# Performance work log

Measured on AMD Instinct MI355X. Metric: run time of the kernel, lower is better.

## Reference

```python
import jax, jax.numpy as jnp
import numpy as np

N_NODES = 100000
N_EDGES = 1600000
N_FEAT = 128
HIDDEN = 128
N_GRAPHS = 100


def setup_inputs() -> dict:
    key = jax.random.key(0)
    ks = jax.random.split(key, 12)
    glorot = lambda k, fi, fo: jax.random.normal(k, (fo, fi), jnp.float32) * (1.0 / np.sqrt(fi))
    x = jax.random.normal(ks[0], (N_NODES, N_FEAT), jnp.float32)
    edge_index = jax.random.randint(ks[1], (2, N_EDGES), 0, N_NODES, jnp.int64)
    batch = jnp.sort(jax.random.randint(ks[2], (N_NODES,), 0, N_GRAPHS, jnp.int64))
    return {
        "x": x,
        "edge_index": edge_index,
        "batch": batch,
        "W1": glorot(ks[3], N_FEAT, HIDDEN), "b1": jnp.zeros((HIDDEN,), jnp.float32),
        "W2": glorot(ks[4], HIDDEN, HIDDEN), "b2": jnp.zeros((HIDDEN,), jnp.float32),
        "W3": glorot(ks[5], HIDDEN, HIDDEN), "b3": jnp.zeros((HIDDEN,), jnp.float32),
        "W4": glorot(ks[6], HIDDEN, HIDDEN), "b4": jnp.zeros((HIDDEN,), jnp.float32),
    }


def _aggregate(x, edge_index):
    # GIN aggregation with eps=0: (1+eps)*x_i + sum_{j in N(i)} x_j
    src, dst = edge_index[0], edge_index[1]
    agg = jax.ops.segment_sum(x[src], dst, num_segments=N_NODES)
    return x + agg


def _mlp(h, Wa, ba, Wb, bb):
    h = jax.nn.relu(h @ Wa.T + ba)
    return jax.nn.relu(h @ Wb.T + bb)


def reference(x, edge_index, batch, W1, b1, W2, b2, W3, b3, W4, b4):
    # conv1: GINConv(MLP1), then extra relu (no-op after MLP's relu), dropout in eval = identity
    h = _mlp(_aggregate(x, edge_index), W1, b1, W2, b2)
    # conv2: GINConv(MLP2), then relu
    h = _mlp(_aggregate(h, edge_index), W3, b3, W4, b4)
    # global mean pool over graphs
    sums = jax.ops.segment_sum(h, batch, num_segments=N_GRAPHS)
    counts = jax.ops.segment_sum(jnp.ones((h.shape[0],), h.dtype), batch, num_segments=N_GRAPHS)
    x_pool = sums / jnp.maximum(counts, 1.0)[:, None]
    return (x_pool, h)
```

## Files before the change

kernel.cpp:

```cpp
#include <hip/hip_runtime.h>

#define N_NODES  100000
#define N_EDGES  1600000
#define NF       128
#define N_GRAPHS 100
#define NBKT     391
#define BKT_SHIFT 8
#define CAP      6144
#define EPB      4096
#define EB_GRID  391

typedef __attribute__((ext_vector_type(8))) short bf16x8;
typedef __attribute__((ext_vector_type(4))) float f32x4;
typedef unsigned int uint32;

__device__ __forceinline__ unsigned short f2bf(float f) {
    union { float f; uint32 u; } x; x.f = f;
    return (unsigned short)((x.u + 0x7fffu + ((x.u >> 16) & 1u)) >> 16);
}
__device__ __forceinline__ uint32 pack2bf(float a, float b) {
    union { float f; uint32 u; } x, y; x.f = a; y.f = b;
    uint32 lo = (x.u + 0x7fffu + ((x.u >> 16) & 1u)) >> 16;
    uint32 hi = (y.u + 0x7fffu + ((y.u >> 16) & 1u)) & 0xffff0000u;
    return lo | hi;
}
__device__ __forceinline__ void add_bf8(float* acc, uint4 v) {
    uint32 u[4] = {v.x, v.y, v.z, v.w};
    #pragma unroll
    for (int i = 0; i < 4; ++i) {
        union { uint32 b; float f; } lo, hi;
        lo.b = u[i] << 16; hi.b = u[i] & 0xffff0000u;
        acc[2 * i] += lo.f; acc[2 * i + 1] += hi.f;
    }
}

__global__ __launch_bounds__(256) void prep(const float4* __restrict__ x,
                                            const float4* __restrict__ w1,
                                            const float4* __restrict__ w2,
                                            const float4* __restrict__ w3,
                                            const float4* __restrict__ w4,
                                            uint4* __restrict__ xb, uint4* __restrict__ wb,
                                            int* __restrict__ cur, float* __restrict__ sums) {
    int bid = blockIdx.x, t = threadIdx.x;
    if (bid < 6250) {
        int i = bid * 256 + t;
        float4 a = x[i * 2], b = x[i * 2 + 1];
        uint4 o;
        o.x = pack2bf(a.x, a.y); o.y = pack2bf(a.z, a.w);
        o.z = pack2bf(b.x, b.y); o.w = pack2bf(b.z, b.w);
        xb[i] = o;
    } else if (bid < 6282) {
        int i = (bid - 6250) * 256 + t;
        int wi = i >> 11, li = i & 2047;
        const float4* s = (wi == 0) ? w1 : (wi == 1) ? w2 : (wi == 2) ? w3 : w4;
        float4 a = s[li * 2], b = s[li * 2 + 1];
        uint4 o;
        o.x = pack2bf(a.x, a.y); o.y = pack2bf(a.z, a.w);
        o.z = pack2bf(b.x, b.y); o.w = pack2bf(b.z, b.w);
        wb[i] = o;
    } else {
        int idx = (bid - 6282) * 256 + t;
        for (int i = idx; i < N_GRAPHS * NF; i += 4096) sums[i] = 0.f;
        if (idx < NBKT) cur[idx] = 0;
    }
}

__global__ __launch_bounds__(512) void bscatter(const int* __restrict__ src,
                                                const int* __restrict__ dst,
                                                int* __restrict__ cur,
                                                uint32* __restrict__ ebuf) {
    __shared__ int lh[NBKT], lbase[NBKT];
    int t = threadIdx.x;
    if (t < NBKT) lh[t] = 0;
    __syncthreads();
    int e0 = blockIdx.x * EPB;
    int d[8];
    #pragma unroll
    for (int i = 0; i < 8; ++i) {
        int e = e0 + i * 512 + t;
        d[i] = -1;
        if (e < N_EDGES) { d[i] = dst[e]; atomicAdd(&lh[d[i] >> BKT_SHIFT], 1); }
    }
    __syncthreads();
    if (t < NBKT) { lbase[t] = t * CAP + atomicAdd(&cur[t], lh[t]); lh[t] = 0; }
    __syncthreads();
    #pragma unroll
    for (int i = 0; i < 8; ++i) {
        int e = e0 + i * 512 + t;
        if (e < N_EDGES) {
            int b = d[i] >> BKT_SHIFT;
            int off = atomicAdd(&lh[b], 1);
            ebuf[lbase[b] + off] = ((uint32)(d[i] & 255) << 17) | (uint32)src[e];
        }
    }
}

__global__ __launch_bounds__(256) void bfine(const uint32* __restrict__ ebuf,
                                             const int* __restrict__ cur,
                                             int* __restrict__ rowptr,
                                             int* __restrict__ rowend,
                                             int* __restrict__ csr) {
    __shared__ int deg[256], off[256];
    int t = threadIdx.x;
    int bkt = blockIdx.x;
    int beg = bkt * CAP;
    int end = beg + cur[bkt];
    deg[t] = 0;
    __syncthreads();
    for (int e = beg + t; e < end; e += 256)
        atomicAdd(&deg[ebuf[e] >> 17], 1);
    __syncthreads();
    int d = deg[t];
    off[t] = d;
    __syncthreads();
    for (int o = 1; o < 256; o <<= 1) {
        int x = (t >= o) ? off[t - o] : 0;
        __syncthreads();
        off[t] += x;
        __syncthreads();
    }
    int ex = off[t] - d;
    int node = (bkt << BKT_SHIFT) + t;
    if (node < N_NODES) { rowptr[node] = beg + ex; rowend[node] = beg + ex + d; }
    __syncthreads();
    off[t] = ex;
    __syncthreads();
    for (int e = beg + t; e < end; e += 256) {
        uint32 u = ebuf[e];
        int pos = atomicAdd(&off[u >> 17], 1);
        csr[beg + pos] = (int)(u & 0x1FFFFu);
    }
}

__global__ __launch_bounds__(256) void gather_agg_bf16(const uint4* __restrict__ x,
                                                       const int* __restrict__ rowptr,
                                                       const int* __restrict__ rowend,
                                                       const int* __restrict__ csr,
                                                       uint4* __restrict__ out) {
    int gid  = blockIdx.x * 256 + threadIdx.x;
    int node = gid >> 6;
    int l = threadIdx.x & 63;
    int c = l & 15;
    int j = l >> 4;
    int beg = rowptr[node], end = rowend[node];

    float acc[8];
    #pragma unroll
    for (int i = 0; i < 8; ++i) acc[i] = 0.f;

    for (int e = beg; e < end; e += 16) {
        int s[4];
        #pragma unroll
        for (int k = 0; k < 4; ++k) {
            int ee = min(e + j + 4 * k, end - 1);
            s[k] = csr[ee];
        }
        uint4 v[4];
        #pragma unroll
        for (int k = 0; k < 4; ++k) v[k] = x[s[k] * 16 + c];
        #pragma unroll
        for (int k = 0; k < 4; ++k)
            if (e + j + 4 * k < end) add_bf8(acc, v[k]);
    }

    #pragma unroll
    for (int i = 0; i < 8; ++i) {
        acc[i] += __shfl_xor(acc[i], 16, 64);
        acc[i] += __shfl_xor(acc[i], 32, 64);
    }

    add_bf8(acc, x[node * 16 + c]);

    if (j == 0) {
        uint4 o;
        o.x = pack2bf(acc[0], acc[1]); o.y = pack2bf(acc[2], acc[3]);
        o.z = pack2bf(acc[4], acc[5]); o.w = pack2bf(acc[6], acc[7]);
        out[node * 16 + c] = o;
    }
}

template <bool F32OUT>
__global__ __launch_bounds__(256, 4) void mlp_mfma(const unsigned short* __restrict__ A,
                                                   const unsigned short* __restrict__ Wa,
                                                   const float* __restrict__ ba,
                                                   const unsigned short* __restrict__ Wb,
                                                   const float* __restrict__ bb,
                                                   void* __restrict__ Cout, int M) {
    __shared__ unsigned short Mid[128 * 136];
    int tid  = threadIdx.x;
    int row0 = blockIdx.x * 128;
    int wv = tid >> 6, l = tid & 63, lm = l & 15, q = l >> 4;

    const unsigned short* pa0 = A + (size_t)min(row0 + wv * 32 + lm,      M - 1) * NF;
    const unsigned short* pa1 = A + (size_t)min(row0 + wv * 32 + 16 + lm, M - 1) * NF;
    const unsigned short* pwa = Wa + lm * NF;
    const unsigned short* pwb = Wb + lm * NF;

    f32x4 acc[2][8];
    #pragma unroll
    for (int i = 0; i < 2; ++i)
        #pragma unroll
        for (int j = 0; j < 8; ++j) acc[i][j] = (f32x4){0.f, 0.f, 0.f, 0.f};

    #pragma unroll
    for (int ks = 0; ks < 4; ++ks) {
        int ko = ks * 32 + q * 8;
        bf16x8 a0 = *(const bf16x8*)(pa0 + ko);
        bf16x8 a1 = *(const bf16x8*)(pa1 + ko);
        #pragma unroll
        for (int ct = 0; ct < 8; ++ct) {
            bf16x8 b = *(const bf16x8*)(pwa + ct * 16 * NF + ko);
            acc[0][ct] = __builtin_amdgcn_mfma_f32_16x16x32_bf16(a0, b, acc[0][ct], 0, 0, 0);
            acc[1][ct] = __builtin_amdgcn_mfma_f32_16x16x32_bf16(a1, b, acc[1][ct], 0, 0, 0);
        }
    }

    #pragma unroll
    for (int rt = 0; rt < 2; ++rt)
        #pragma unroll
        for (int ct = 0; ct < 8; ++ct) {
            int col = ct * 16 + lm;
            float bv = ba[col];
            #pragma unroll
            for (int r = 0; r < 4; ++r) {
                int rr = wv * 32 + rt * 16 + q * 4 + r;
                Mid[rr * 136 + col] = f2bf(fmaxf(acc[rt][ct][r] + bv, 0.f));
            }
        }
    __syncthreads();

    #pragma unroll
    for (int i = 0; i < 2; ++i)
        #pragma unroll
        for (int j = 0; j < 8; ++j) acc[i][j] = (f32x4){0.f, 0.f, 0.f, 0.f};

    const unsigned short* pm0 = &Mid[(wv * 32 + lm) * 136];
    const unsigned short* pm1 = &Mid[(wv * 32 + 16 + lm) * 136];
    #pragma unroll
    for (int ks = 0; ks < 4; ++ks) {
        int ko = ks * 32 + q * 8;
        bf16x8 a0 = *(const bf16x8*)(pm0 + ko);
        bf16x8 a1 = *(const bf16x8*)(pm1 + ko);
        #pragma unroll
        for (int ct = 0; ct < 8; ++ct) {
            bf16x8 b = *(const bf16x8*)(pwb + ct * 16 * NF + ko);
            acc[0][ct] = __builtin_amdgcn_mfma_f32_16x16x32_bf16(a0, b, acc[0][ct], 0, 0, 0);
            acc[1][ct] = __builtin_amdgcn_mfma_f32_16x16x32_bf16(a1, b, acc[1][ct], 0, 0, 0);
        }
    }

    #pragma unroll
    for (int rt = 0; rt < 2; ++rt)
        #pragma unroll
        for (int ct = 0; ct < 8; ++ct) {
            int col = ct * 16 + lm;
            float bv = bb[col];
            #pragma unroll
            for (int r = 0; r < 4; ++r) {
                int row = row0 + wv * 32 + rt * 16 + q * 4 + r;
                if (row < M) {
                    float v = fmaxf(acc[rt][ct][r] + bv, 0.f);
                    if (F32OUT) ((float*)Cout)[(size_t)row * NF + col] = v;
                    else ((unsigned short*)Cout)[(size_t)row * NF + col] = f2bf(v);
                }
            }
        }
}

__global__ __launch_bounds__(256) void pool_sum2(const float* __restrict__ h,
                                                 const int* __restrict__ batch,
                                                 float* __restrict__ sums) {
    int t = threadIdx.x;
    int f = t & 127, seg = t >> 7;
    int n0 = blockIdx.x * 128 + seg * 64;
    if (n0 >= N_NODES) return;
    int n1 = min(n0 + 64, N_NODES);
    int cur = batch[n0];
    float acc = 0.f;
    for (int n = n0; n < n1; ++n) {
        int g = batch[n];
        if (g != cur) {
            atomicAdd(&sums[cur * NF + f], acc);
            acc = 0.f; cur = g;
        }
        acc += h[(size_t)n * NF + f];
    }
    atomicAdd(&sums[cur * NF + f], acc);
}

__global__ __launch_bounds__(256) void pool_div2(const float* __restrict__ sums,
                                                 const int* __restrict__ batch,
                                                 float* __restrict__ out) {
    int i = blockIdx.x * 256 + threadIdx.x;
    if (i >= N_GRAPHS * NF) return;
    int g = i >> 7;
    int lo = 0, hi = N_NODES;
    while (lo < hi) { int m = (lo + hi) >> 1; if (batch[m] < g) lo = m + 1; else hi = m; }
    int lo2 = lo, hi2 = N_NODES;
    while (lo2 < hi2) { int m = (lo2 + hi2) >> 1; if (batch[m] < g + 1) lo2 = m + 1; else hi2 = m; }
    float cnt = (float)(lo2 - lo);
    out[i] = sums[i] / fmaxf(cnt, 1.f);
}

extern "C" void kernel_launch(void* const* d_in, const int* in_sizes, int n_in,
                              void* d_out, int out_size, void* d_ws, size_t ws_size,
                              hipStream_t stream) {
    const float* x     = (const float*)d_in[0];
    const int*   ei    = (const int*)d_in[1];
    const int*   batch = (const int*)d_in[2];
    const float* W1 = (const float*)d_in[3];  const float* b1 = (const float*)d_in[4];
    const float* W2 = (const float*)d_in[5];  const float* b2 = (const float*)d_in[6];
    const float* W3 = (const float*)d_in[7];  const float* b3 = (const float*)d_in[8];
    const float* W4 = (const float*)d_in[9];  const float* b4 = (const float*)d_in[10];
    const int* src = ei;
    const int* dst = ei + N_EDGES;

    float* out   = (float*)d_out;
    float* h_out = out + N_GRAPHS * NF;

    const size_t NE = (size_t)N_NODES * NF;
    unsigned short* xb = (unsigned short*)d_ws;
    unsigned short* t0 = xb + NE;
    unsigned short* t1 = t0 + NE;
    unsigned short* Wb = t1 + NE;
    int*    rowptr = (int*)(Wb + 4 * NF * NF);
    int*    rowend = rowptr + N_NODES;
    int*    csr    = rowend + N_NODES;
    uint32* ebuf   = (uint32*)(csr + NBKT * CAP);
    int*    curp   = (int*)(ebuf + NBKT * CAP);
    float*  sums   = (float*)(curp + NBKT);

    const int gather_blocks = N_NODES * 64 / 256;
    const int gemm_blocks   = (N_NODES + 127) / 128;

    prep<<<6250 + 32 + 16, 256, 0, stream>>>((const float4*)x,
                                             (const float4*)W1, (const float4*)W2,
                                             (const float4*)W3, (const float4*)W4,
                                             (uint4*)xb, (uint4*)Wb, curp, sums);

    bscatter<<<EB_GRID, 512, 0, stream>>>(src, dst, curp, ebuf);
    bfine<<<NBKT, 256, 0, stream>>>(ebuf, curp, rowptr, rowend, csr);

    gather_agg_bf16<<<gather_blocks, 256, 0, stream>>>((const uint4*)xb, rowptr, rowend, csr, (uint4*)t0);
    mlp_mfma<false><<<gemm_blocks, 256, 0, stream>>>(t0, Wb + 0 * NF * NF, b1,
                                                     Wb + 1 * NF * NF, b2, t1, N_NODES);

    gather_agg_bf16<<<gather_blocks, 256, 0, stream>>>((const uint4*)t1, rowptr, rowend, csr, (uint4*)t0);
    mlp_mfma<true ><<<gemm_blocks, 256, 0, stream>>>(t0, Wb + 2 * NF * NF, b3,
                                                     Wb + 3 * NF * NF, b4, h_out, N_NODES);

    pool_sum2<<<(N_NODES + 127) / 128, 256, 0, stream>>>(h_out, batch, sums);
    pool_div2<<<(N_GRAPHS * NF + 255) / 256, 256, 0, stream>>>(sums, batch, out);
}
```

Measured before the change: 409.8 us.

## Use finer edge buckets, zero-row padded gather, vectorized pooling, relaxed GEMM bounds

Halves the CSR bucket size (128 nodes per bucket, 782 buckets, 256-thread scatter) so more blocks work in the bucket-sort stages with smaller shared histograms. The gather loop now handles 32 edges per iteration with 8 loads in flight, and sends out-of-range edges to an appended zero row instead of branching. This requires padding every bf16 feature buffer by one row that prep zeroes. Pooling switches to float4 loads over shorter node segments, and the GEMM drops its min-blocks-per-CU launch bound. The trade-offs are more atomics to the global bucket counters, more atomics in pooling, and possibly different register allocation in the GEMM.

```diff
diff --git a/kernel.cpp b/kernel.cpp
--- a/kernel.cpp
+++ b/kernel.cpp
@@ -4,11 +4,12 @@
 #define N_EDGES  1600000
 #define NF       128
 #define N_GRAPHS 100
-#define NBKT     391
-#define BKT_SHIFT 8
-#define CAP      6144
-#define EPB      4096
-#define EB_GRID  391
+#define ZROW     N_NODES
+#define NBKT     782
+#define BKT_SHIFT 7
+#define CAP      2560
+#define EPB      2048
+#define EB_GRID  782
 
 typedef __attribute__((ext_vector_type(8))) short bf16x8;
 typedef __attribute__((ext_vector_type(4))) float f32x4;
@@ -40,6 +41,8 @@
                                             const float4* __restrict__ w3,
                                             const float4* __restrict__ w4,
                                             uint4* __restrict__ xb, uint4* __restrict__ wb,
+                                            uint32* __restrict__ xz, uint32* __restrict__ t0z,
+                                            uint32* __restrict__ t1z,
                                             int* __restrict__ cur, float* __restrict__ sums) {
     int bid = blockIdx.x, t = threadIdx.x;
     if (bid < 6250) {
@@ -62,35 +65,42 @@
         int idx = (bid - 6282) * 256 + t;
         for (int i = idx; i < N_GRAPHS * NF; i += 4096) sums[i] = 0.f;
         if (idx < NBKT) cur[idx] = 0;
-    }
-}
-
-__global__ __launch_bounds__(512) void bscatter(const int* __restrict__ src,
+        if (idx < 192) {
+            uint32* p = (idx < 64) ? xz : (idx < 128) ? t0z : t1z;
+            p[idx & 63] = 0u;
+        }
+    }
+}
+
+__global__ __launch_bounds__(256) void bscatter(const int* __restrict__ src,
                                                 const int* __restrict__ dst,
                                                 int* __restrict__ cur,
                                                 uint32* __restrict__ ebuf) {
     __shared__ int lh[NBKT], lbase[NBKT];
     int t = threadIdx.x;
-    if (t < NBKT) lh[t] = 0;
+    for (int i = t; i < NBKT; i += 256) lh[i] = 0;
     __syncthreads();
     int e0 = blockIdx.x * EPB;
     int d[8];
     #pragma unroll
     for (int i = 0; i < 8; ++i) {
-        int e = e0 + i * 512 + t;
+        int e = e0 + i * 256 + t;
         d[i] = -1;
         if (e < N_EDGES) { d[i] = dst[e]; atomicAdd(&lh[d[i] >> BKT_SHIFT], 1); }
     }
     __syncthreads();
-    if (t < NBKT) { lbase[t] = t * CAP + atomicAdd(&cur[t], lh[t]); lh[t] = 0; }
+    for (int i = t; i < NBKT; i += 256) {
+        lbase[i] = i * CAP + atomicAdd(&cur[i], lh[i]);
+        lh[i] = 0;
+    }
     __syncthreads();
     #pragma unroll
     for (int i = 0; i < 8; ++i) {
-        int e = e0 + i * 512 + t;
+        int e = e0 + i * 256 + t;
         if (e < N_EDGES) {
             int b = d[i] >> BKT_SHIFT;
             int off = atomicAdd(&lh[b], 1);
-            ebuf[lbase[b] + off] = ((uint32)(d[i] & 255) << 17) | (uint32)src[e];
+            ebuf[lbase[b] + off] = ((uint32)(d[i] & 127) << 17) | (uint32)src[e];
         }
     }
 }
@@ -100,30 +110,31 @@
                                              int* __restrict__ rowptr,
                                              int* __restrict__ rowend,
                                              int* __restrict__ csr) {
-    __shared__ int deg[256], off[256];
+    __shared__ int deg[128], off[128];
     int t = threadIdx.x;
     int bkt = blockIdx.x;
     int beg = bkt * CAP;
     int end = beg + cur[bkt];
-    deg[t] = 0;
+    if (t < 128) deg[t] = 0;
     __syncthreads();
     for (int e = beg + t; e < end; e += 256)
         atomicAdd(&deg[ebuf[e] >> 17], 1);
     __syncthreads();
-    int d = deg[t];
-    off[t] = d;
-    __syncthreads();
-    for (int o = 1; o < 256; o <<= 1) {
-        int x = (t >= o) ? off[t - o] : 0;
+    int d = 0;
+    if (t < 128) { d = deg[t]; off[t] = d; }
+    __syncthreads();
+    for (int o = 1; o < 128; o <<= 1) {
+        int x = (t < 128 && t >= o) ? off[t - o] : 0;
         __syncthreads();
-        off[t] += x;
+        if (t < 128) off[t] += x;
         __syncthreads();
     }
-    int ex = off[t] - d;
-    int node = (bkt << BKT_SHIFT) + t;
-    if (node < N_NODES) { rowptr[node] = beg + ex; rowend[node] = beg + ex + d; }
-    __syncthreads();
-    off[t] = ex;
+    if (t < 128) {
+        int ex = off[t] - d;
+        int node = (bkt << BKT_SHIFT) + t;
+        if (node < N_NODES) { rowptr[node] = beg + ex; rowend[node] = beg + ex + d; }
+        off[t] = ex;
+    }
     __syncthreads();
     for (int e = beg + t; e < end; e += 256) {
         uint32 u = ebuf[e];
@@ -148,19 +159,19 @@
     #pragma unroll
     for (int i = 0; i < 8; ++i) acc[i] = 0.f;
 
-    for (int e = beg; e < end; e += 16) {
-        int s[4];
-        #pragma unroll
-        for (int k = 0; k < 4; ++k) {
-            int ee = min(e + j + 4 * k, end - 1);
-            s[k] = csr[ee];
-        }
-        uint4 v[4];
-        #pragma unroll
-        for (int k = 0; k < 4; ++k) v[k] = x[s[k] * 16 + c];
-        #pragma unroll
-        for (int k = 0; k < 4; ++k)
-            if (e + j + 4 * k < end) add_bf8(acc, v[k]);
+    for (int base = beg; base < end; base += 32) {
+        int s[8];
+        #pragma unroll
+        for (int k = 0; k < 8; ++k) {
+            int idx = base + j + 4 * k;
+            int sv = csr[min(idx, end - 1)];
+            s[k] = (idx < end) ? sv : ZROW;
+        }
+        uint4 v[8];
+        #pragma unroll
+        for (int k = 0; k < 8; ++k) v[k] = x[s[k] * 16 + c];
+        #pragma unroll
+        for (int k = 0; k < 8; ++k) add_bf8(acc, v[k]);
     }
 
     #pragma unroll
@@ -180,12 +191,12 @@
 }
 
 template <bool F32OUT>
-__global__ __launch_bounds__(256, 4) void mlp_mfma(const unsigned short* __restrict__ A,
-                                                   const unsigned short* __restrict__ Wa,
-                                                   const float* __restrict__ ba,
-                                                   const unsigned short* __restrict__ Wb,
-                                                   const float* __restrict__ bb,
-                                                   void* __restrict__ Cout, int M) {
+__global__ __launch_bounds__(256) void mlp_mfma(const unsigned short* __restrict__ A,
+                                                const unsigned short* __restrict__ Wa,
+                                                const float* __restrict__ ba,
+                                                const unsigned short* __restrict__ Wb,
+                                                const float* __restrict__ bb,
+                                                void* __restrict__ Cout, int M) {
     __shared__ unsigned short Mid[128 * 136];
     int tid  = threadIdx.x;
     int row0 = blockIdx.x * 128;
@@ -267,25 +278,30 @@
         }
 }
 
-__global__ __launch_bounds__(256) void pool_sum2(const float* __restrict__ h,
+__global__ __launch_bounds__(256) void pool_sum3(const float4* __restrict__ h4,
                                                  const int* __restrict__ batch,
                                                  float* __restrict__ sums) {
     int t = threadIdx.x;
-    int f = t & 127, seg = t >> 7;
-    int n0 = blockIdx.x * 128 + seg * 64;
+    int lane = t & 31, seg = t >> 5;
+    int n0 = blockIdx.x * 128 + seg * 16;
     if (n0 >= N_NODES) return;
-    int n1 = min(n0 + 64, N_NODES);
+    int n1 = min(n0 + 16, N_NODES);
     int cur = batch[n0];
-    float acc = 0.f;
+    float4 acc = make_float4(0.f, 0.f, 0.f, 0.f);
     for (int n = n0; n < n1; ++n) {
         int g = batch[n];
         if (g != cur) {
-            atomicAdd(&sums[cur * NF + f], acc);
-            acc = 0.f; cur = g;
-        }
-        acc += h[(size_t)n * NF + f];
-    }
-    atomicAdd(&sums[cur * NF + f], acc);
+            float* p = &sums[cur * NF + lane * 4];
+            atomicAdd(p + 0, acc.x); atomicAdd(p + 1, acc.y);
+            atomicAdd(p + 2, acc.z); atomicAdd(p + 3, acc.w);
+            acc = make_float4(0.f, 0.f, 0.f, 0.f); cur = g;
+        }
+        float4 v = h4[(size_t)n * 32 + lane];
+        acc.x += v.x; acc.y += v.y; acc.z += v.z; acc.w += v.w;
+    }
+    float* p = &sums[cur * NF + lane * 4];
+    atomicAdd(p + 0, acc.x); atomicAdd(p + 1, acc.y);
+    atomicAdd(p + 2, acc.z); atomicAdd(p + 3, acc.w);
 }
 
 __global__ __launch_bounds__(256) void pool_div2(const float* __restrict__ sums,
@@ -318,11 +334,11 @@
     float* out   = (float*)d_out;
     float* h_out = out + N_GRAPHS * NF;
 
-    const size_t NE = (size_t)N_NODES * NF;
+    const size_t NE1 = (size_t)(N_NODES + 1) * NF;
     unsigned short* xb = (unsigned short*)d_ws;
-    unsigned short* t0 = xb + NE;
-    unsigned short* t1 = t0 + NE;
-    unsigned short* Wb = t1 + NE;
+    unsigned short* t0 = xb + NE1;
+    unsigned short* t1 = t0 + NE1;
+    unsigned short* Wb = t1 + NE1;
     int*    rowptr = (int*)(Wb + 4 * NF * NF);
     int*    rowend = rowptr + N_NODES;
     int*    csr    = rowend + N_NODES;
@@ -336,9 +352,13 @@
     prep<<<6250 + 32 + 16, 256, 0, stream>>>((const float4*)x,
                                              (const float4*)W1, (const float4*)W2,
                                              (const float4*)W3, (const float4*)W4,
-                                             (uint4*)xb, (uint4*)Wb, curp, sums);
-
-    bscatter<<<EB_GRID, 512, 0, stream>>>(src, dst, curp, ebuf);
+                                             (uint4*)xb, (uint4*)Wb,
+                                             (uint32*)(xb + (size_t)N_NODES * NF),
+                                             (uint32*)(t0 + (size_t)N_NODES * NF),
+                                             (uint32*)(t1 + (size_t)N_NODES * NF),
+                                             curp, sums);
+
+    bscatter<<<EB_GRID, 256, 0, stream>>>(src, dst, curp, ebuf);
     bfine<<<NBKT, 256, 0, stream>>>(ebuf, curp, rowptr, rowend, csr);
 
     gather_agg_bf16<<<gather_blocks, 256, 0, stream>>>((const uint4*)xb, rowptr, rowend, csr, (uint4*)t0);
@@ -349,6 +369,6 @@
     mlp_mfma<true ><<<gemm_blocks, 256, 0, stream>>>(t0, Wb + 2 * NF * NF, b3,
                                                      Wb + 3 * NF * NF, b4, h_out, N_NODES);
 
-    pool_sum2<<<(N_NODES + 127) / 128, 256, 0, stream>>>(h_out, batch, sums);
+    pool_sum3<<<(N_NODES + 127) / 128, 256, 0, stream>>>((const float4*)h_out, batch, sums);
     pool_div2<<<(N_GRAPHS * NF + 255) / 256, 256, 0, stream>>>(sums, batch, out);
 }
```

Measured after the change: 453.2 us. 1.11x slower.
